# Kernel tuning notes

Measured on AMD Instinct MI355X. Metric: run time of the kernel, lower is better.

The kernel has to match this reference:

```python
import jax, jax.numpy as jnp
import numpy as np

B, N, D, H = 2, 512, 256, 256  # batch, seq_len, input_dim, hidden_dim
H2 = H // 2


def setup_inputs() -> dict:
    key = jax.random.key(0)
    ks = jax.random.split(key, 12)
    def lin(kw, kb, fan_in, fan_out):
        bound = 1.0 / np.sqrt(fan_in)
        W = jax.random.uniform(kw, (fan_in, fan_out), jnp.float32, -bound, bound)
        b = jax.random.uniform(kb, (fan_out,), jnp.float32, -bound, bound)
        return W, b
    W1, b1 = lin(ks[0], ks[1], 2 * D, H)
    W2, b2 = lin(ks[2], ks[3], H, H2)
    W3, b3 = lin(ks[4], ks[5], H2, 1)
    Wg, bg = lin(ks[6], ks[7], D, H)
    x = jax.random.normal(ks[8], (B, N, D), jnp.float32)
    base_adj = jax.random.uniform(ks[9], (B, N, N), jnp.float32)
    return {"x": x, "base_adj": base_adj, "W1": W1, "b1": b1,
            "W2": W2, "b2": b2, "W3": W3, "b3": b3, "Wg": Wg, "bg": bg}


def reference(x, base_adj, W1, b1, W2, b2, W3, b3, Wg, bg):
    # x: [B,N,D], base_adj: [B,N,N]
    Din = x.shape[-1]
    n = x.shape[1]
    # Linear on concat([x_i, x_j]) == x_i @ W1[:D] + x_j @ W1[D:]  (same math,
    # avoids materializing the [B,N,N,2D] pair tensor)
    left = jnp.einsum('bid,dh->bih', x, W1[:Din])    # [B,N,H]
    right = jnp.einsum('bjd,dh->bjh', x, W1[Din:])   # [B,N,H]
    h = jax.nn.relu(left[:, :, None, :] + right[:, None, :, :] + b1)  # [B,N,N,H]
    h = jax.nn.relu(jnp.einsum('bijh,hk->bijk', h, W2) + b2)          # [B,N,N,H/2]
    edge_weights = jax.nn.sigmoid(jnp.einsum('bijk,k->bij', h, W3[:, 0]) + b3[0])
    dynamic_adj = base_adj * edge_weights + jnp.eye(n, dtype=x.dtype)[None]
    dynamic_adj = jax.nn.softmax(dynamic_adj, axis=-1)
    agg = jnp.matmul(dynamic_adj, x)                 # [B,N,D]
    return jnp.einsum('bnd,dh->bnh', agg, Wg) + bg   # [B,N,H]
```

## Files before the change

### kernel.cpp

```cpp
#include <hip/hip_runtime.h>
#include <hip/hip_bf16.h>

#define NB 2
#define NN 512
#define ND 256
#define NH 256
#define NH2 128
#define JT 32

typedef __bf16 bf16x8 __attribute__((ext_vector_type(8)));
typedef __bf16 bf16x4 __attribute__((ext_vector_type(4)));
typedef float f32x4 __attribute__((ext_vector_type(4)));

__device__ __forceinline__ void gload_lds16(const void* g, void* l) {
  __builtin_amdgcn_global_load_lds((const __attribute__((address_space(1))) unsigned int*)g,
                                   (__attribute__((address_space(3))) unsigned int*)l, 16, 0, 0);
}
__device__ __forceinline__ float bflo(unsigned d) { return __uint_as_float(d << 16); }
__device__ __forceinline__ float bfhi(unsigned d) { return __uint_as_float(d & 0xffff0000u); }

__global__ __launch_bounds__(256) void prep_kernel(
    const float* __restrict__ x, const float* __restrict__ W1,
    const float* __restrict__ b1, const float* __restrict__ Wg,
    const float* __restrict__ bg, const float* __restrict__ W2,
    float* __restrict__ Lb, __bf16* __restrict__ Rb16,
    __bf16* __restrict__ XWb16, __bf16* __restrict__ W2b) {
  const int blk = blockIdx.x;
  const int tid = threadIdx.x;
  if (blk >= 512) {
    const int idx = (blk - 512) * 256 + tid;
    const int h = idx >> 7;
    const int k = idx & 127;
    W2b[k * NH + h] = (__bf16)W2[idx];
    return;
  }
  __shared__ float xs[2][ND];
  __shared__ __align__(16) f32x4 part[4 * 384];
  const int r0 = blk * 2;
  xs[0][tid] = x[r0 * ND + tid];
  xs[1][tid] = x[(r0 + 1) * ND + tid];
  __syncthreads();

  const int dg = tid >> 6;
  const int hq = tid & 63;
  f32x4 acc[2][3];
  #pragma unroll
  for (int r = 0; r < 2; ++r)
    #pragma unroll
    for (int m = 0; m < 3; ++m) acc[r][m] = (f32x4){0.f, 0.f, 0.f, 0.f};

  const int d0 = dg * 64;
  for (int it = 0; it < 64; ++it) {
    const int d = d0 + it;
    const f32x4 wl = *(const f32x4*)(W1 + d * NH + hq * 4);
    const f32x4 wr = *(const f32x4*)(W1 + (ND + d) * NH + hq * 4);
    const f32x4 wg = *(const f32x4*)(Wg + d * NH + hq * 4);
    const float x0 = xs[0][d], x1 = xs[1][d];
    acc[0][0] += x0 * wl;  acc[0][1] += x0 * wr;  acc[0][2] += x0 * wg;
    acc[1][0] += x1 * wl;  acc[1][1] += x1 * wr;  acc[1][2] += x1 * wg;
  }
  #pragma unroll
  for (int r = 0; r < 2; ++r)
    #pragma unroll
    for (int m = 0; m < 3; ++m)
      part[dg * 384 + (r * 3 + m) * 64 + hq] = acc[r][m];
  __syncthreads();

  for (int s = tid; s < 384; s += 256) {
    f32x4 sum = part[s] + part[384 + s] + part[768 + s] + part[1152 + s];
    const int r = s / 192;
    const int rem = s - r * 192;
    const int m = rem >> 6;
    const int h = (rem & 63) * 4;
    const int row = r0 + r;
    if (m == 0) {
      const f32x4 bv = *(const f32x4*)(b1 + h);
      *(f32x4*)(Lb + row * NH + h) = sum + bv;
    } else if (m == 1) {
      bf16x4 o;
      #pragma unroll
      for (int e = 0; e < 4; ++e) o[e] = (__bf16)sum[e];
      *(bf16x4*)(Rb16 + row * NH + h) = o;
    } else {
      const f32x4 bv = *(const f32x4*)(bg + h);
      const f32x4 v = sum + bv;
      bf16x4 o;
      #pragma unroll
      for (int e = 0; e < 4; ++e) o[e] = (__bf16)v[e];
      *(bf16x4*)(XWb16 + row * NH + h) = o;
    }
  }
}

__global__ __launch_bounds__(256, 4) void edge_kernel(
    const float* __restrict__ base_adj,
    const float* __restrict__ b2, const float* __restrict__ W3,
    const float* __restrict__ b3, const float* __restrict__ Lb,
    const __bf16* __restrict__ Rb16, const __bf16* __restrict__ XWb16,
    const __bf16* __restrict__ W2b, float* __restrict__ out) {
  __shared__ __align__(16) __bf16 Rs[JT * NH];
  __shared__ __align__(16) __bf16 Hs[JT * NH];
  __shared__ __align__(16) float Lbs[NH];
  __shared__ float adjs[NN];
  __shared__ float ew[NN];
  __shared__ float red[4][JT];
  __shared__ float b2s[NH2], W3s[NH2];
  __shared__ float sred[8];

  const int bi = blockIdx.x;
  const int b = bi >> 9;
  const int i = bi & (NN - 1);
  const int tid = threadIdx.x;
  const int lane = tid & 63;
  const int w = tid >> 6;
  const int lr = lane & 15;
  const int lg = lane >> 4;

  const __bf16* Rbb = Rb16 + b * NN * NH;

  {
    const int laneoff = (lane >> 5) * NH + (lane & 31) * 8;
    #pragma unroll
    for (int q = 0; q < 4; ++q) {
      const __bf16* src = Rbb + (w * 4 + q) * 2 * NH + laneoff;
      gload_lds16(src, (char*)Rs + (w * 4 + q) * 1024);
    }
  }
  bf16x8 bfr[8][2];
  #pragma unroll
  for (int ks8 = 0; ks8 < 8; ++ks8)
    #pragma unroll
    for (int kb = 0; kb < 2; ++kb) {
      const int k = w * 32 + kb * 16 + lr;
      bfr[ks8][kb] = *(const bf16x8*)(W2b + k * NH + ks8 * 32 + lg * 8);
    }
  Lbs[tid] = Lb[bi * NH + tid];
  adjs[tid] = base_adj[(b * NN + i) * NN + tid];
  adjs[tid + 256] = base_adj[(b * NN + i) * NN + tid + 256];
  if (tid < NH2) { b2s[tid] = b2[tid]; W3s[tid] = W3[tid]; }
  const float b3v = b3[0];
  asm volatile("s_waitcnt vmcnt(0)" ::: "memory");
  __syncthreads();

  const int cth = tid & 31;
  float l8[8];
  #pragma unroll
  for (int e = 0; e < 8; ++e) l8[e] = Lbs[cth * 8 + e];
  const int rowth = tid >> 5;
  const unsigned rsAddr0 = tid * 16;
  const unsigned hsAddr0 = rowth * 512 + ((cth ^ (rowth & 7)) << 4);

  for (int jt = 0; jt < 16; ++jt) {
    #pragma unroll
    for (int it = 0; it < 4; ++it) {
      const uint4 rv = *(const uint4*)((const char*)Rs + rsAddr0 + it * 4096);
      bf16x8 hb;
      #pragma unroll
      for (int e = 0; e < 4; ++e) {
        const unsigned d = ((const unsigned*)&rv)[e];
        float t0 = bflo(d) + l8[2 * e];
        float t1 = bfhi(d) + l8[2 * e + 1];
        t0 = t0 > 0.f ? t0 : 0.f;
        t1 = t1 > 0.f ? t1 : 0.f;
        hb[2 * e] = (__bf16)t0;
        hb[2 * e + 1] = (__bf16)t1;
      }
      *(bf16x8*)((char*)Hs + hsAddr0 + it * 4096) = hb;
    }
    __syncthreads();

    if (jt < 15) {
      const int laneoff = (lane >> 5) * NH + (lane & 31) * 8;
      const __bf16* base = Rbb + (jt + 1) * (JT * NH);
      #pragma unroll
      for (int q = 0; q < 4; ++q) {
        const __bf16* src = base + (w * 4 + q) * 2 * NH + laneoff;
        gload_lds16(src, (char*)Rs + (w * 4 + q) * 1024);
      }
    }

    f32x4 acc[2][2];
    #pragma unroll
    for (int ja = 0; ja < 2; ++ja)
      #pragma unroll
      for (int kb = 0; kb < 2; ++kb) acc[ja][kb] = (f32x4){0.f, 0.f, 0.f, 0.f};
    #pragma unroll
    for (int ks8 = 0; ks8 < 8; ++ks8) {
      bf16x8 af[2];
      #pragma unroll
      for (int ja = 0; ja < 2; ++ja) {
        const int row = ja * 16 + lr;
        const int c = (ks8 * 4 + lg) ^ (lr & 7);
        af[ja] = *(const bf16x8*)((const char*)Hs + row * 512 + (c << 4));
      }
      #pragma unroll
      for (int ja = 0; ja < 2; ++ja)
        #pragma unroll
        for (int kb = 0; kb < 2; ++kb)
          acc[ja][kb] = __builtin_amdgcn_mfma_f32_16x16x32_bf16(af[ja], bfr[ks8][kb], acc[ja][kb], 0, 0, 0);
    }

    #pragma unroll
    for (int ja = 0; ja < 2; ++ja) {
      #pragma unroll
      for (int r = 0; r < 4; ++r) {
        const int k0 = w * 32 + lr;
        float t0 = acc[ja][0][r] + b2s[k0];
        float t1 = acc[ja][1][r] + b2s[k0 + 16];
        t0 = t0 > 0.f ? t0 : 0.f;
        t1 = t1 > 0.f ? t1 : 0.f;
        float s = fmaf(t0, W3s[k0], t1 * W3s[k0 + 16]);
        s += __shfl_xor(s, 1, 16);
        s += __shfl_xor(s, 2, 16);
        s += __shfl_xor(s, 4, 16);
        s += __shfl_xor(s, 8, 16);
        if (lr == 0) red[w][ja * 16 + lg * 4 + r] = s;
      }
    }
    asm volatile("s_waitcnt vmcnt(0)" ::: "memory");
    __syncthreads();

    if (tid < JT) {
      const float v = red[0][tid] + red[1][tid] + red[2][tid] + red[3][tid] + b3v;
      const float sg = 1.f / (1.f + __expf(-v));
      const int j = jt * JT + tid;
      ew[j] = adjs[j] * sg + ((j == i) ? 1.f : 0.f);
    }
  }
  __syncthreads();

  float v0 = ew[tid], v1 = ew[tid + 256];
  float m = fmaxf(v0, v1);
  #pragma unroll
  for (int off = 1; off < 64; off <<= 1) m = fmaxf(m, __shfl_xor(m, off, 64));
  if (lane == 0) sred[w] = m;
  __syncthreads();
  m = fmaxf(fmaxf(sred[0], sred[1]), fmaxf(sred[2], sred[3]));
  const float e0 = __expf(v0 - m), e1 = __expf(v1 - m);
  float ssum = e0 + e1;
  #pragma unroll
  for (int off = 1; off < 64; off <<= 1) ssum += __shfl_xor(ssum, off, 64);
  if (lane == 0) sred[4 + w] = ssum;
  __syncthreads();
  const float inv = 1.f / (sred[4] + sred[5] + sred[6] + sred[7]);
  ew[tid] = e0 * inv;
  ew[tid + 256] = e1 * inv;
  __syncthreads();

  const int jg = tid >> 7;
  const int h2 = tid & 127;
  const unsigned* Xp = (const unsigned*)(XWb16 + b * NN * NH) + jg * 256 * 128 + h2;
  float a0 = 0.f, a1 = 0.f, c0 = 0.f, c1 = 0.f;
  for (int jj = 0; jj < 256; jj += 2) {
    const int j0 = jg * 256 + jj;
    const unsigned d0 = Xp[jj * 128];
    const unsigned d1 = Xp[jj * 128 + 128];
    const float p0 = ew[j0], p1 = ew[j0 + 1];
    a0 = fmaf(p0, bflo(d0), a0);  a1 = fmaf(p0, bfhi(d0), a1);
    c0 = fmaf(p1, bflo(d1), c0);  c1 = fmaf(p1, bfhi(d1), c1);
  }
  float* pv = adjs;
  pv[jg * 256 + h2 * 2] = a0 + c0;
  pv[jg * 256 + h2 * 2 + 1] = a1 + c1;
  __syncthreads();
  out[bi * NH + tid] = pv[tid] + pv[256 + tid];
}

extern "C" void kernel_launch(void* const* d_in, const int* in_sizes, int n_in,
                              void* d_out, int out_size, void* d_ws, size_t ws_size,
                              hipStream_t stream) {
  const float* x        = (const float*)d_in[0];
  const float* base_adj = (const float*)d_in[1];
  const float* W1       = (const float*)d_in[2];
  const float* b1       = (const float*)d_in[3];
  const float* W2       = (const float*)d_in[4];
  const float* b2       = (const float*)d_in[5];
  const float* W3       = (const float*)d_in[6];
  const float* b3       = (const float*)d_in[7];
  const float* Wg       = (const float*)d_in[8];
  const float* bg       = (const float*)d_in[9];

  float*  Lb    = (float*)d_ws;
  __bf16* Rb16  = (__bf16*)(Lb + NB * NN * NH);
  __bf16* XWb16 = Rb16 + NB * NN * NH;
  __bf16* W2b   = XWb16 + NB * NN * NH;
  float* outp = (float*)d_out;

  prep_kernel<<<640, 256, 0, stream>>>(x, W1, b1, Wg, bg, W2, Lb, Rb16, XWb16, W2b);
  edge_kernel<<<NB * NN, 256, 0, stream>>>(base_adj, b2, W3, b3, Lb, Rb16, XWb16, W2b, outp);
}
```

Before: 163.3 us.

## Fuse prep and edge kernels with grid barrier, double-buffer H, MFMA aggregation

Merges the projection prep kernel into the edge kernel using an atomic grid-wide barrier, which removes a second launch. The R tiles now go through registers with a double-buffered H tile in LDS in place of the global-to-LDS async loads. The final softmax-weighted aggregation now runs on MFMA, using a split hi/lo bf16 representation of the probabilities against a transposed XW. This adds a memset launch and relies on all 1024 blocks being co-resident for the spin barrier, which risks deadlock and adds a spin wait.

```diff
diff --git a/kernel.cpp b/kernel.cpp
--- a/kernel.cpp
+++ b/kernel.cpp
@@ -12,173 +12,167 @@
 typedef __bf16 bf16x4 __attribute__((ext_vector_type(4)));
 typedef float f32x4 __attribute__((ext_vector_type(4)));
 
-__device__ __forceinline__ void gload_lds16(const void* g, void* l) {
-  __builtin_amdgcn_global_load_lds((const __attribute__((address_space(1))) unsigned int*)g,
-                                   (__attribute__((address_space(3))) unsigned int*)l, 16, 0, 0);
-}
 __device__ __forceinline__ float bflo(unsigned d) { return __uint_as_float(d << 16); }
 __device__ __forceinline__ float bfhi(unsigned d) { return __uint_as_float(d & 0xffff0000u); }
 
-__global__ __launch_bounds__(256) void prep_kernel(
-    const float* __restrict__ x, const float* __restrict__ W1,
-    const float* __restrict__ b1, const float* __restrict__ Wg,
-    const float* __restrict__ bg, const float* __restrict__ W2,
-    float* __restrict__ Lb, __bf16* __restrict__ Rb16,
-    __bf16* __restrict__ XWb16, __bf16* __restrict__ W2b) {
-  const int blk = blockIdx.x;
-  const int tid = threadIdx.x;
-  if (blk >= 512) {
-    const int idx = (blk - 512) * 256 + tid;
-    const int h = idx >> 7;
-    const int k = idx & 127;
-    W2b[k * NH + h] = (__bf16)W2[idx];
-    return;
-  }
-  __shared__ float xs[2][ND];
-  __shared__ __align__(16) f32x4 part[4 * 384];
-  const int r0 = blk * 2;
-  xs[0][tid] = x[r0 * ND + tid];
-  xs[1][tid] = x[(r0 + 1) * ND + tid];
-  __syncthreads();
-
-  const int dg = tid >> 6;
-  const int hq = tid & 63;
-  f32x4 acc[2][3];
-  #pragma unroll
-  for (int r = 0; r < 2; ++r)
-    #pragma unroll
-    for (int m = 0; m < 3; ++m) acc[r][m] = (f32x4){0.f, 0.f, 0.f, 0.f};
-
-  const int d0 = dg * 64;
-  for (int it = 0; it < 64; ++it) {
-    const int d = d0 + it;
-    const f32x4 wl = *(const f32x4*)(W1 + d * NH + hq * 4);
-    const f32x4 wr = *(const f32x4*)(W1 + (ND + d) * NH + hq * 4);
-    const f32x4 wg = *(const f32x4*)(Wg + d * NH + hq * 4);
-    const float x0 = xs[0][d], x1 = xs[1][d];
-    acc[0][0] += x0 * wl;  acc[0][1] += x0 * wr;  acc[0][2] += x0 * wg;
-    acc[1][0] += x1 * wl;  acc[1][1] += x1 * wr;  acc[1][2] += x1 * wg;
-  }
-  #pragma unroll
-  for (int r = 0; r < 2; ++r)
-    #pragma unroll
-    for (int m = 0; m < 3; ++m)
-      part[dg * 384 + (r * 3 + m) * 64 + hq] = acc[r][m];
-  __syncthreads();
-
-  for (int s = tid; s < 384; s += 256) {
-    f32x4 sum = part[s] + part[384 + s] + part[768 + s] + part[1152 + s];
-    const int r = s / 192;
-    const int rem = s - r * 192;
-    const int m = rem >> 6;
-    const int h = (rem & 63) * 4;
-    const int row = r0 + r;
-    if (m == 0) {
-      const f32x4 bv = *(const f32x4*)(b1 + h);
-      *(f32x4*)(Lb + row * NH + h) = sum + bv;
-    } else if (m == 1) {
-      bf16x4 o;
-      #pragma unroll
-      for (int e = 0; e < 4; ++e) o[e] = (__bf16)sum[e];
-      *(bf16x4*)(Rb16 + row * NH + h) = o;
-    } else {
-      const f32x4 bv = *(const f32x4*)(bg + h);
-      const f32x4 v = sum + bv;
-      bf16x4 o;
-      #pragma unroll
-      for (int e = 0; e < 4; ++e) o[e] = (__bf16)v[e];
-      *(bf16x4*)(XWb16 + row * NH + h) = o;
-    }
+__device__ __forceinline__ void buildHs(char* dst, const uint4* rg4, const float* l8,
+                                        unsigned hsOff) {
+  #pragma unroll
+  for (int it = 0; it < 4; ++it) {
+    const uint4 rv = rg4[it];
+    bf16x8 hb;
+    #pragma unroll
+    for (int e = 0; e < 4; ++e) {
+      const unsigned d = ((const unsigned*)&rv)[e];
+      float t0 = bflo(d) + l8[2 * e];
+      float t1 = bfhi(d) + l8[2 * e + 1];
+      t0 = t0 > 0.f ? t0 : 0.f;
+      t1 = t1 > 0.f ? t1 : 0.f;
+      hb[2 * e] = (__bf16)t0;
+      hb[2 * e + 1] = (__bf16)t1;
+    }
+    *(bf16x8*)(dst + hsOff + it * 4096) = hb;
   }
 }
 
-__global__ __launch_bounds__(256, 4) void edge_kernel(
-    const float* __restrict__ base_adj,
-    const float* __restrict__ b2, const float* __restrict__ W3,
-    const float* __restrict__ b3, const float* __restrict__ Lb,
-    const __bf16* __restrict__ Rb16, const __bf16* __restrict__ XWb16,
-    const __bf16* __restrict__ W2b, float* __restrict__ out) {
-  __shared__ __align__(16) __bf16 Rs[JT * NH];
-  __shared__ __align__(16) __bf16 Hs[JT * NH];
-  __shared__ __align__(16) float Lbs[NH];
-  __shared__ float adjs[NN];
-  __shared__ float ew[NN];
-  __shared__ float red[4][JT];
+__global__ __launch_bounds__(256, 4) void fused_kernel(
+    const float* __restrict__ x, const float* __restrict__ base_adj,
+    const float* __restrict__ W1, const float* __restrict__ b1,
+    const float* __restrict__ W2, const float* __restrict__ b2,
+    const float* __restrict__ W3, const float* __restrict__ b3,
+    const float* __restrict__ Wg, const float* __restrict__ bg,
+    unsigned* __restrict__ bar, float* __restrict__ Lb,
+    __bf16* __restrict__ Rb16, __bf16* __restrict__ XWt,
+    __bf16* __restrict__ W2b, float* __restrict__ out) {
+  __shared__ __align__(16) char ovl[32768];
+  __shared__ __align__(16) float adjs[NN];
+  __shared__ __align__(16) float ew[NN];
+  __shared__ float red[2][4][JT];
   __shared__ float b2s[NH2], W3s[NH2];
   __shared__ float sred[8];
 
-  const int bi = blockIdx.x;
-  const int b = bi >> 9;
-  const int i = bi & (NN - 1);
+  const int blk = blockIdx.x;
   const int tid = threadIdx.x;
   const int lane = tid & 63;
   const int w = tid >> 6;
   const int lr = lane & 15;
   const int lg = lane >> 4;
-
-  const __bf16* Rbb = Rb16 + b * NN * NH;
-
-  {
-    const int laneoff = (lane >> 5) * NH + (lane & 31) * 8;
-    #pragma unroll
-    for (int q = 0; q < 4; ++q) {
-      const __bf16* src = Rbb + (w * 4 + q) * 2 * NH + laneoff;
-      gload_lds16(src, (char*)Rs + (w * 4 + q) * 1024);
-    }
-  }
-  bf16x8 bfr[8][2];
-  #pragma unroll
-  for (int ks8 = 0; ks8 < 8; ++ks8)
-    #pragma unroll
-    for (int kb = 0; kb < 2; ++kb) {
-      const int k = w * 32 + kb * 16 + lr;
-      bfr[ks8][kb] = *(const bf16x8*)(W2b + k * NH + ks8 * 32 + lg * 8);
-    }
-  Lbs[tid] = Lb[bi * NH + tid];
+  const int b = blk >> 9;
+  const int i = blk & (NN - 1);
+
   adjs[tid] = base_adj[(b * NN + i) * NN + tid];
   adjs[tid + 256] = base_adj[(b * NN + i) * NN + tid + 256];
   if (tid < NH2) { b2s[tid] = b2[tid]; W3s[tid] = W3[tid]; }
   const float b3v = b3[0];
-  asm volatile("s_waitcnt vmcnt(0)" ::: "memory");
-  __syncthreads();
+
+  {
+    const int rg = blk >> 4;
+    const int hg = blk & 15;
+    const int r0 = rg * 16;
+    const int h0 = hg * 16;
+    float* xs = (float*)ovl;
+    f32x4* part = (f32x4*)(ovl + 16 * 260 * 4);
+    #pragma unroll
+    for (int s = tid; s < 16 * 256; s += 256)
+      xs[(s >> 8) * 260 + (s & 255)] = x[(r0 + (s >> 8)) * ND + (s & 255)];
+    if (tid < 32) {
+      const int idx = blk * 32 + tid;
+      const int hh = idx >> 7, kk = idx & 127;
+      W2b[kk * NH + hh] = (__bf16)W2[idx];
+    }
+    __syncthreads();
+
+    const int item = tid & 63;
+    const int dg = tid >> 6;
+    const int rl = item >> 2;
+    const int h4 = h0 + (item & 3) * 4;
+    f32x4 aL = {0.f,0.f,0.f,0.f}, aR = {0.f,0.f,0.f,0.f}, aG = {0.f,0.f,0.f,0.f};
+    const float* xr = xs + rl * 260 + dg * 64;
+    #pragma unroll 4
+    for (int it = 0; it < 64; ++it) {
+      const int d = dg * 64 + it;
+      const f32x4 wl = *(const f32x4*)(W1 + d * NH + h4);
+      const f32x4 wr = *(const f32x4*)(W1 + (ND + d) * NH + h4);
+      const f32x4 wg = *(const f32x4*)(Wg + d * NH + h4);
+      const float xv = xr[it];
+      aL += xv * wl; aR += xv * wr; aG += xv * wg;
+    }
+    part[dg * 192 + item * 3 + 0] = aL;
+    part[dg * 192 + item * 3 + 1] = aR;
+    part[dg * 192 + item * 3 + 2] = aG;
+    __syncthreads();
+
+    if (tid < 192) {
+      const f32x4 sum = part[tid] + part[192 + tid] + part[384 + tid] + part[576 + tid];
+      const int it2 = tid / 3;
+      const int m = tid - it2 * 3;
+      const int row = r0 + (it2 >> 2);
+      const int hh4 = h0 + (it2 & 3) * 4;
+      if (m == 0) {
+        *(f32x4*)(Lb + row * NH + hh4) = sum + *(const f32x4*)(b1 + hh4);
+      } else if (m == 1) {
+        bf16x4 o;
+        #pragma unroll
+        for (int e = 0; e < 4; ++e) o[e] = (__bf16)sum[e];
+        *(bf16x4*)(Rb16 + row * NH + hh4) = o;
+      } else {
+        const f32x4 v = sum + *(const f32x4*)(bg + hh4);
+        const int bb = row >> 9, jj = row & (NN - 1);
+        #pragma unroll
+        for (int e = 0; e < 4; ++e)
+          XWt[bb * (NH * NN) + (hh4 + e) * NN + jj] = (__bf16)v[e];
+      }
+    }
+  }
+
+  __threadfence();
+  __syncthreads();
+  if (tid == 0) {
+    __hip_atomic_fetch_add(bar, 1u, __ATOMIC_ACQ_REL, __HIP_MEMORY_SCOPE_AGENT);
+    while (__hip_atomic_load(bar, __ATOMIC_ACQUIRE, __HIP_MEMORY_SCOPE_AGENT) <
+           (unsigned)gridDim.x) {
+      __builtin_amdgcn_s_sleep(2);
+    }
+  }
+  __syncthreads();
+  __threadfence();
+
+  const __bf16* Rbb = Rb16 + b * NN * NH;
+  const __bf16* XWtb = XWt + b * NH * NN;
+  char* HsB = ovl;
 
   const int cth = tid & 31;
+  const int rowth = tid >> 5;
+  const unsigned hsOff = rowth * 512 + ((cth ^ (rowth & 7)) << 4);
+
   float l8[8];
-  #pragma unroll
-  for (int e = 0; e < 8; ++e) l8[e] = Lbs[cth * 8 + e];
-  const int rowth = tid >> 5;
-  const unsigned rsAddr0 = tid * 16;
-  const unsigned hsAddr0 = rowth * 512 + ((cth ^ (rowth & 7)) << 4);
+  {
+    const f32x4 la = *(const f32x4*)(Lb + blk * NH + cth * 8);
+    const f32x4 lc = *(const f32x4*)(Lb + blk * NH + cth * 8 + 4);
+    #pragma unroll
+    for (int e = 0; e < 4; ++e) { l8[e] = la[e]; l8[4 + e] = lc[e]; }
+  }
+
+  bf16x8 bfr[8][2];
+  #pragma unroll
+  for (int ks8 = 0; ks8 < 8; ++ks8)
+    #pragma unroll
+    for (int kb = 0; kb < 2; ++kb)
+      bfr[ks8][kb] = *(const bf16x8*)(W2b + (w * 32 + kb * 16 + lr) * NH + ks8 * 32 + lg * 8);
+
+  uint4 rg4[4];
+  #pragma unroll
+  for (int it = 0; it < 4; ++it)
+    rg4[it] = *(const uint4*)(Rbb + (it * 8 + rowth) * NH + cth * 8);
+  buildHs(HsB, rg4, l8, hsOff);
+  #pragma unroll
+  for (int it = 0; it < 4; ++it)
+    rg4[it] = *(const uint4*)(Rbb + (JT + it * 8 + rowth) * NH + cth * 8);
+  __syncthreads();
 
   for (int jt = 0; jt < 16; ++jt) {
-    #pragma unroll
-    for (int it = 0; it < 4; ++it) {
-      const uint4 rv = *(const uint4*)((const char*)Rs + rsAddr0 + it * 4096);
-      bf16x8 hb;
-      #pragma unroll
-      for (int e = 0; e < 4; ++e) {
-        const unsigned d = ((const unsigned*)&rv)[e];
-        float t0 = bflo(d) + l8[2 * e];
-        float t1 = bfhi(d) + l8[2 * e + 1];
-        t0 = t0 > 0.f ? t0 : 0.f;
-        t1 = t1 > 0.f ? t1 : 0.f;
-        hb[2 * e] = (__bf16)t0;
-        hb[2 * e + 1] = (__bf16)t1;
-      }
-      *(bf16x8*)((char*)Hs + hsAddr0 + it * 4096) = hb;
-    }
-    __syncthreads();
-
-    if (jt < 15) {
-      const int laneoff = (lane >> 5) * NH + (lane & 31) * 8;
-      const __bf16* base = Rbb + (jt + 1) * (JT * NH);
-      #pragma unroll
-      for (int q = 0; q < 4; ++q) {
-        const __bf16* src = base + (w * 4 + q) * 2 * NH + laneoff;
-        gload_lds16(src, (char*)Rs + (w * 4 + q) * 1024);
-      }
-    }
-
+    const int buf = jt & 1;
+    const char* Hp = HsB + buf * 16384;
     f32x4 acc[2][2];
     #pragma unroll
     for (int ja = 0; ja < 2; ++ja)
@@ -188,18 +182,14 @@
     for (int ks8 = 0; ks8 < 8; ++ks8) {
       bf16x8 af[2];
       #pragma unroll
-      for (int ja = 0; ja < 2; ++ja) {
-        const int row = ja * 16 + lr;
-        const int c = (ks8 * 4 + lg) ^ (lr & 7);
-        af[ja] = *(const bf16x8*)((const char*)Hs + row * 512 + (c << 4));
-      }
+      for (int ja = 0; ja < 2; ++ja)
+        af[ja] = *(const bf16x8*)(Hp + (ja * 16 + lr) * 512 + (((ks8 * 4 + lg) ^ (lr & 7)) << 4));
       #pragma unroll
       for (int ja = 0; ja < 2; ++ja)
         #pragma unroll
         for (int kb = 0; kb < 2; ++kb)
           acc[ja][kb] = __builtin_amdgcn_mfma_f32_16x16x32_bf16(af[ja], bfr[ks8][kb], acc[ja][kb], 0, 0, 0);
     }
-
     #pragma unroll
     for (int ja = 0; ja < 2; ++ja) {
       #pragma unroll
@@ -214,14 +204,19 @@
         s += __shfl_xor(s, 2, 16);
         s += __shfl_xor(s, 4, 16);
         s += __shfl_xor(s, 8, 16);
-        if (lr == 0) red[w][ja * 16 + lg * 4 + r] = s;
+        if (lr == 0) red[buf][w][ja * 16 + lg * 4 + r] = s;
       }
     }
-    asm volatile("s_waitcnt vmcnt(0)" ::: "memory");
+    if (jt < 15) buildHs(HsB + (buf ^ 1) * 16384, rg4, l8, hsOff);
+    if (jt < 14) {
+      #pragma unroll
+      for (int it = 0; it < 4; ++it)
+        rg4[it] = *(const uint4*)(Rbb + ((jt + 2) * JT + it * 8 + rowth) * NH + cth * 8);
+    }
     __syncthreads();
-
     if (tid < JT) {
-      const float v = red[0][tid] + red[1][tid] + red[2][tid] + red[3][tid] + b3v;
+      const float v = red[buf][0][tid] + red[buf][1][tid] + red[buf][2][tid] +
+                      red[buf][3][tid] + b3v;
       const float sg = 1.f / (1.f + __expf(-v));
       const int j = jt * JT + tid;
       ew[j] = adjs[j] * sg + ((j == i) ? 1.f : 0.f);
@@ -243,27 +238,41 @@
   if (lane == 0) sred[4 + w] = ssum;
   __syncthreads();
   const float inv = 1.f / (sred[4] + sred[5] + sred[6] + sred[7]);
-  ew[tid] = e0 * inv;
-  ew[tid + 256] = e1 * inv;
-  __syncthreads();
-
-  const int jg = tid >> 7;
-  const int h2 = tid & 127;
-  const unsigned* Xp = (const unsigned*)(XWb16 + b * NN * NH) + jg * 256 * 128 + h2;
-  float a0 = 0.f, a1 = 0.f, c0 = 0.f, c1 = 0.f;
-  for (int jj = 0; jj < 256; jj += 2) {
-    const int j0 = jg * 256 + jj;
-    const unsigned d0 = Xp[jj * 128];
-    const unsigned d1 = Xp[jj * 128 + 128];
-    const float p0 = ew[j0], p1 = ew[j0 + 1];
-    a0 = fmaf(p0, bflo(d0), a0);  a1 = fmaf(p0, bfhi(d0), a1);
-    c0 = fmaf(p1, bflo(d1), c0);  c1 = fmaf(p1, bfhi(d1), c1);
-  }
-  float* pv = adjs;
-  pv[jg * 256 + h2 * 2] = a0 + c0;
-  pv[jg * 256 + h2 * 2 + 1] = a1 + c1;
-  __syncthreads();
-  out[bi * NH + tid] = pv[tid] + pv[256 + tid];
+  const float p0 = e0 * inv, p1 = e1 * inv;
+
+  __bf16* ewh = (__bf16*)ew;
+  __bf16* ewl = ewh + NN;
+  {
+    const __bf16 h0 = (__bf16)p0;
+    const __bf16 h1 = (__bf16)p1;
+    ewh[tid] = h0;        ewl[tid] = (__bf16)(p0 - (float)h0);
+    ewh[tid + 256] = h1;  ewl[tid + 256] = (__bf16)(p1 - (float)h1);
+  }
+  __syncthreads();
+
+  const char* ewb = (const char*)ew;
+  const unsigned aoff = (lr == 1 ? 1024u : 0u) + lg * 16;
+  const bool azero = (lr >= 2);
+  f32x4 pacc[4];
+  #pragma unroll
+  for (int q = 0; q < 4; ++q) pacc[q] = (f32x4){0.f, 0.f, 0.f, 0.f};
+  #pragma unroll
+  for (int ks = 0; ks < 16; ++ks) {
+    uint4 pa = *(const uint4*)(ewb + aoff + ks * 64);
+    if (azero) { pa.x = 0; pa.y = 0; pa.z = 0; pa.w = 0; }
+    const bf16x8 paf = __builtin_bit_cast(bf16x8, pa);
+    #pragma unroll
+    for (int q = 0; q < 4; ++q) {
+      const int h = w * 64 + q * 16 + lr;
+      const bf16x8 bv = *(const bf16x8*)(XWtb + h * NN + ks * 32 + lg * 8);
+      pacc[q] = __builtin_amdgcn_mfma_f32_16x16x32_bf16(paf, bv, pacc[q], 0, 0, 0);
+    }
+  }
+  if (lg == 0) {
+    #pragma unroll
+    for (int q = 0; q < 4; ++q)
+      out[blk * NH + w * 64 + q * 16 + lr] = pacc[q][0] + pacc[q][1];
+  }
 }
 
 extern "C" void kernel_launch(void* const* d_in, const int* in_sizes, int n_in,
@@ -280,12 +289,14 @@
   const float* Wg       = (const float*)d_in[8];
   const float* bg       = (const float*)d_in[9];
 
-  float*  Lb    = (float*)d_ws;
+  unsigned* bar = (unsigned*)d_ws;
+  float*  Lb    = (float*)((char*)d_ws + 64);
   __bf16* Rb16  = (__bf16*)(Lb + NB * NN * NH);
-  __bf16* XWb16 = Rb16 + NB * NN * NH;
-  __bf16* W2b   = XWb16 + NB * NN * NH;
+  __bf16* XWt   = Rb16 + NB * NN * NH;
+  __bf16* W2b   = XWt + NB * NH * NN;
   float* outp = (float*)d_out;
 
-  prep_kernel<<<640, 256, 0, stream>>>(x, W1, b1, Wg, bg, W2, Lb, Rb16, XWb16, W2b);
-  edge_kernel<<<NB * NN, 256, 0, stream>>>(base_adj, b2, W3, b3, Lb, Rb16, XWb16, W2b, outp);
+  hipMemsetAsync(bar, 0, 64, stream);
+  fused_kernel<<<NB * NN, 256, 0, stream>>>(x, base_adj, W1, b1, W2, b2, W3, b3,
+                                            Wg, bg, bar, Lb, Rb16, XWt, W2b, outp);
 }
```

After: 517.0 us. 217% more time.
